# Optimization experiments

Measured on AMD Instinct MI355X. Metric: run time of the kernel, lower is better.

The kernel has to match this reference:

```python
import jax, jax.numpy as jnp
import numpy as np

N, E, G = 50000, 1600000, 64
F_NODE, F_EDGE, ACT = 128, 16, 10
NEG_SLOPE = 0.2  # GATv2Conv default negative_slope
LAYER_DIMS = [(F_NODE, 32), (32, 64), (64, 128)]


def _glorot(k, shape):
    fan_in, fan_out = shape[0], shape[-1]
    s = jnp.sqrt(6.0 / (fan_in + fan_out))
    return jax.random.uniform(k, shape, jnp.float32, -s, s)


def setup_inputs() -> dict:
    key = jax.random.key(0)
    ks = iter(jax.random.split(key, 64))
    inp = {
        "x": jax.random.normal(next(ks), (N, F_NODE), jnp.float32),
        "edge_attr": jax.random.normal(next(ks), (E, F_EDGE), jnp.float32),
        "edge_index": jax.random.randint(next(ks), (2, E), 0, N, jnp.int32),
        "batch": jnp.sort(jax.random.randint(next(ks), (N,), 0, G, jnp.int32)),
    }
    for i, (din, dout) in enumerate(LAYER_DIMS, 1):
        inp[f"Wl{i}"] = _glorot(next(ks), (din, dout))   # lin_l (source transform)
        inp[f"bl{i}"] = jnp.zeros((dout,), jnp.float32)
        inp[f"Wr{i}"] = _glorot(next(ks), (din, dout))   # lin_r (dest transform)
        inp[f"br{i}"] = jnp.zeros((dout,), jnp.float32)
        inp[f"We{i}"] = _glorot(next(ks), (F_EDGE, dout))  # lin_edge (no bias)
        inp[f"att{i}"] = _glorot(next(ks), (1, dout))[0]   # attention vector
        inp[f"bo{i}"] = jnp.zeros((dout,), jnp.float32)    # output bias
    inp["Wv1"] = _glorot(next(ks), (128, 64)); inp["bv1"] = jnp.zeros((64,), jnp.float32)
    inp["Wv2"] = _glorot(next(ks), (64, 1));   inp["bv2"] = jnp.zeros((1,), jnp.float32)
    inp["Wa1"] = _glorot(next(ks), (128, 64)); inp["ba1"] = jnp.zeros((64,), jnp.float32)
    inp["Wa2"] = _glorot(next(ks), (64, ACT)); inp["ba2"] = jnp.zeros((ACT,), jnp.float32)
    return inp


def _gatv2(x, src, dst, ea, Wl, bl, Wr, br, We, att, bo):
    """GATv2Conv, heads=1, concat=True, edge_dim=F_EDGE (eval mode)."""
    xl = x @ Wl + bl                               # [N, D] source-side
    xr = x @ Wr + br                               # [N, D] dest-side
    m = xl[src] + xr[dst] + ea @ We                # [E, D]
    score = (jax.nn.leaky_relu(m, NEG_SLOPE) * att).sum(-1)  # [E]
    # segment softmax over edges grouped by destination node
    mx = jax.lax.stop_gradient(jax.ops.segment_max(score, dst, num_segments=N))
    ex = jnp.exp(score - mx[dst])
    den = jax.ops.segment_sum(ex, dst, num_segments=N)
    alpha = ex / (den[dst] + 1e-16)                # [E]
    out = jax.ops.segment_sum(alpha[:, None] * xl[src], dst, num_segments=N)
    return out + bo


def _forward(x, edge_attr, src, dst, batch, p):
    h = x
    for i in (1, 2, 3):
        h = jax.nn.relu(_gatv2(h, src, dst, edge_attr,
                               p[f"Wl{i}"], p[f"bl{i}"], p[f"Wr{i}"], p[f"br{i}"],
                               p[f"We{i}"], p[f"att{i}"], p[f"bo{i}"]))
    # global mean pool per graph
    cnt = jax.ops.segment_sum(jnp.ones((N,), h.dtype), batch, num_segments=G)
    pooled = jax.ops.segment_sum(h, batch, num_segments=G) / jnp.maximum(cnt, 1.0)[:, None]
    # dueling heads
    v = jax.nn.relu(pooled @ p["Wv1"] + p["bv1"]) @ p["Wv2"] + p["bv2"]      # [G, 1]
    a = jax.nn.relu(pooled @ p["Wa1"] + p["ba1"]) @ p["Wa2"] + p["ba2"]      # [G, ACT]
    return v + (a - a.mean(axis=1, keepdims=True))


def reference(x, edge_attr, edge_index, batch,
              Wl1, bl1, Wr1, br1, We1, att1, bo1,
              Wl2, bl2, Wr2, br2, We2, att2, bo2,
              Wl3, bl3, Wr3, br3, We3, att3, bo3,
              Wv1, bv1, Wv2, bv2, Wa1, ba1, Wa2, ba2):
    p = dict(Wl1=Wl1, bl1=bl1, Wr1=Wr1, br1=br1, We1=We1, att1=att1, bo1=bo1,
             Wl2=Wl2, bl2=bl2, Wr2=Wr2, br2=br2, We2=We2, att2=att2, bo2=bo2,
             Wl3=Wl3, bl3=bl3, Wr3=Wr3, br3=br3, We3=We3, att3=att3, bo3=bo3,
             Wv1=Wv1, bv1=bv1, Wv2=Wv2, bv2=bv2, Wa1=Wa1, ba1=ba1, Wa2=Wa2, ba2=ba2)
    return _forward(x, edge_attr, edge_index[0], edge_index[1], batch, p)
```

## Files before the change

kernel.cpp:

```cpp
#include <hip/hip_runtime.h>
#include <cstdint>
#include <cstddef>

static constexpr int NN = 50000;
static constexpr int NE = 1600000;
static constexpr int NG = 64;
static constexpr int FE = 16;
static constexpr float SLOPE = 0.2f;

template<int DIN, int DOUT>
__global__ __launch_bounds__(256) void k_node_linear(
    const float* __restrict__ h,
    const float* __restrict__ Wl, const float* __restrict__ bl,
    const float* __restrict__ Wr, const float* __restrict__ br,
    float* __restrict__ xl, float* __restrict__ xr)
{
    __shared__ float sW[2 * DIN * DOUT];
    __shared__ float sX[16 * DIN];
    const int n0 = blockIdx.x * 16;

    for (int i = threadIdx.x; i < DIN * DOUT; i += 256) {
        sW[i] = Wl[i];
        sW[DIN * DOUT + i] = Wr[i];
    }
    for (int i = threadIdx.x; i < 16 * DIN; i += 256) {
        int r = i / DIN, k = i % DIN;
        int n = n0 + r;
        sX[i] = (n < NN) ? h[(size_t)n * DIN + k] : 0.0f;
    }
    __syncthreads();

    for (int o = threadIdx.x; o < 16 * DOUT; o += 256) {
        int r = o / DOUT, d = o % DOUT;
        int n = n0 + r;
        if (n >= NN) continue;
        float accl = bl[d], accr = br[d];
        #pragma unroll 8
        for (int k = 0; k < DIN; ++k) {
            float xv = sX[r * DIN + k];
            accl = fmaf(xv, sW[k * DOUT + d], accl);
            accr = fmaf(xv, sW[DIN * DOUT + k * DOUT + d], accr);
        }
        xl[(size_t)n * DOUT + d] = accl;
        xr[(size_t)n * DOUT + d] = accr;
    }
}

__global__ __launch_bounds__(256) void k_count(
    const int* __restrict__ ei, int* __restrict__ cnt)
{
    const int e = blockIdx.x * 256 + threadIdx.x;
    if (e >= NE) return;
    atomicAdd(cnt + ei[NE + e], 1);
}

__global__ __launch_bounds__(1024) void k_scan(
    const int* __restrict__ cnt, int* __restrict__ rowptr)
{
    __shared__ int part[1024];
    const int T = 1024;
    const int C = (NN + T - 1) / T;
    const int t = threadIdx.x;
    const int base = t * C;
    int s = 0;
    for (int i = 0; i < C; ++i) {
        int idx = base + i;
        if (idx < NN) s += cnt[idx];
    }
    part[t] = s;
    __syncthreads();
    for (int off = 1; off < T; off <<= 1) {
        int v = 0;
        if (t >= off) v = part[t - off];
        __syncthreads();
        if (t >= off) part[t] += v;
        __syncthreads();
    }
    int run = (t == 0) ? 0 : part[t - 1];
    for (int i = 0; i < C; ++i) {
        int idx = base + i;
        if (idx < NN) { rowptr[idx] = run; run += cnt[idx]; }
    }
    if (t == T - 1) rowptr[NN] = run;
}

__global__ __launch_bounds__(256) void k_fill(
    const int* __restrict__ ei, const int* __restrict__ rowptr,
    int* __restrict__ woff, int* __restrict__ eids, int* __restrict__ esrc)
{
    const int e = blockIdx.x * 256 + threadIdx.x;
    if (e >= NE) return;
    const int dst = ei[NE + e];
    const int pos = rowptr[dst] + atomicAdd(woff + dst, 1);
    eids[pos] = e;
    esrc[pos] = ei[e];
}

__global__ __launch_bounds__(256) void k_gather_ea(
    const int* __restrict__ eids, const float* __restrict__ ea,
    float* __restrict__ eap)
{
    const long long i = (long long)blockIdx.x * 256 + threadIdx.x;
    if (i >= (long long)NE * 4) return;
    const int p = (int)(i >> 2), q = (int)(i & 3);
    const int e = eids[p];
    *(float4*)(eap + (size_t)p * FE + q * 4) =
        *(const float4*)(ea + (size_t)e * FE + q * 4);
}

template<int D, bool PERM>
__global__ __launch_bounds__(128, 4) void k_gat_fused(
    const int* __restrict__ rowptr, const int* __restrict__ eidx,
    const int* __restrict__ esrc, const float* __restrict__ eaf,
    const float* __restrict__ xl, const float* __restrict__ xr,
    const float* __restrict__ We, const float* __restrict__ att,
    const float* __restrict__ bo, float* __restrict__ hout)
{
    constexpr int SW  = D / 2;
    constexpr int EPW = 64 / SW;
    constexpr int WPB = 2;

    const int wave = threadIdx.x >> 6;
    const int lane = threadIdx.x & 63;
    const int n = blockIdx.x * WPB + wave;
    if (n >= NN) return;
    const int sub = lane / SW;
    const int dl  = lane % SW;
    const int d0  = 2 * dl;

    float rWe[2 * FE], rAtt[2], rXr[2], acc[2];
    {
        const float2 a2 = *(const float2*)(att + d0);
        rAtt[0] = a2.x; rAtt[1] = a2.y;
        const float2 x2 = *(const float2*)(xr + (size_t)n * D + d0);
        rXr[0] = x2.x; rXr[1] = x2.y;
        #pragma unroll
        for (int k = 0; k < FE; ++k) {
            const float2 w2 = *(const float2*)(We + k * D + d0);
            rWe[2 * k] = w2.x; rWe[2 * k + 1] = w2.y;
        }
        acc[0] = acc[1] = 0.f;
    }

    const int p0 = rowptr[n], p1 = rowptr[n + 1];
    float m = -3.4e38f, l = 0.f;

    auto load_edge = [&](int p, float (&eav)[FE], float (&rXl)[2]) {
        const int s = esrc[p];
        const float2 x2 = *(const float2*)(xl + (size_t)s * D + d0);
        rXl[0] = x2.x; rXl[1] = x2.y;
        int erow; if constexpr (PERM) erow = p; else erow = eidx[p];
        if constexpr (SW == 64) {
            const float* ep = eaf + (size_t)(unsigned)__builtin_amdgcn_readfirstlane(erow) * FE;
            #pragma unroll
            for (int k = 0; k < FE; ++k) eav[k] = ep[k];
        } else {
            const float* ep = eaf + (size_t)erow * FE;
            #pragma unroll
            for (int k4 = 0; k4 < 4; ++k4) {
                const float4 v = *(const float4*)(ep + 4 * k4);
                eav[4 * k4]     = v.x; eav[4 * k4 + 1] = v.y;
                eav[4 * k4 + 2] = v.z; eav[4 * k4 + 3] = v.w;
            }
        }
    };
    auto score_edge = [&](const float (&eav)[FE], const float (&rXl)[2]) -> float {
        float m0 = rXl[0] + rXr[0], m1 = rXl[1] + rXr[1];
        #pragma unroll
        for (int k = 0; k < FE; ++k) {
            m0 = fmaf(eav[k], rWe[2 * k], m0);
            m1 = fmaf(eav[k], rWe[2 * k + 1], m1);
        }
        m0 = m0 > 0.f ? m0 : SLOPE * m0;
        m1 = m1 > 0.f ? m1 : SLOPE * m1;
        float sv = fmaf(m0, rAtt[0], m1 * rAtt[1]);
        #pragma unroll
        for (int off = 1; off < SW; off <<= 1) sv += __shfl_xor(sv, off);
        return sv;
    };
    auto sm_update = [&](float sv, const float (&rXl)[2]) {
        const float dd = sv - m;
        float wexp;
        if (__builtin_expect(dd > 8.f, 0)) {
            const float r = __expf(-dd);
            acc[0] *= r; acc[1] *= r;
            l *= r; m = sv; wexp = 1.f;
        } else {
            wexp = __expf(dd);
        }
        acc[0] = fmaf(wexp, rXl[0], acc[0]);
        acc[1] = fmaf(wexp, rXl[1], acc[1]);
        l += wexp;
    };

    int p = p0 + sub;
    for (; p + EPW < p1; p += 2 * EPW) {
        float eavA[FE], rXlA[2], eavB[FE], rXlB[2];
        load_edge(p, eavA, rXlA);
        load_edge(p + EPW, eavB, rXlB);
        const float svA = score_edge(eavA, rXlA);
        const float svB = score_edge(eavB, rXlB);
        sm_update(svA, rXlA);
        sm_update(svB, rXlB);
    }
    if (p < p1) {
        float eav[FE], rXl[2];
        load_edge(p, eav, rXl);
        sm_update(score_edge(eav, rXl), rXl);
    }

    #pragma unroll
    for (int step = SW; step < 64; step <<= 1) {
        const float mo = __shfl_xor(m, step);
        const float mstar = fmaxf(m, mo);
        const float sc = __expf(m - mstar);
        acc[0] *= sc; acc[1] *= sc; l *= sc;
        acc[0] += __shfl_xor(acc[0], step);
        acc[1] += __shfl_xor(acc[1], step);
        l += __shfl_xor(l, step);
        m = mstar;
    }

    if (lane < SW) {
        const float inv = 1.0f / (l + 1e-16f);
        const float2 b2 = *(const float2*)(bo + d0);
        float2 o;
        o.x = fmaxf(fmaf(acc[0], inv, b2.x), 0.f);
        o.y = fmaxf(fmaf(acc[1], inv, b2.y), 0.f);
        *(float2*)(hout + (size_t)n * D + d0) = o;
    }
}

__global__ __launch_bounds__(128) void k_pool(
    const float* __restrict__ h, const int* __restrict__ batch,
    float* __restrict__ pooled, float* __restrict__ cnt)
{
    constexpr int BLOCKS = 512;
    constexpr int CH = (NN + BLOCKS - 1) / BLOCKS;
    const int t = threadIdx.x;
    const int n0 = blockIdx.x * CH;
    const int n1 = min(NN, n0 + CH);
    if (n0 >= n1) return;

    int g = batch[n0];
    float acc = 0.f, c = 0.f;
    for (int n = n0; n < n1; ++n) {
        const int bg = batch[n];
        if (bg != g) {
            atomicAdd(pooled + g * 128 + t, acc);
            if (t == 0) atomicAdd(cnt + g, c);
            acc = 0.f; c = 0.f; g = bg;
        }
        acc += h[(size_t)n * 128 + t];
        c += 1.f;
    }
    atomicAdd(pooled + g * 128 + t, acc);
    if (t == 0) atomicAdd(cnt + g, c);
}

__global__ __launch_bounds__(128) void k_head(
    const float* __restrict__ pooled, const float* __restrict__ cnt,
    const float* __restrict__ Wv1, const float* __restrict__ bv1,
    const float* __restrict__ Wv2, const float* __restrict__ bv2,
    const float* __restrict__ Wa1, const float* __restrict__ ba1,
    const float* __restrict__ Wa2, const float* __restrict__ ba2,
    float* __restrict__ out)
{
    __shared__ float pr[128];
    __shared__ float hv[64];
    __shared__ float ha[64];
    __shared__ float sA[10];
    __shared__ float sVM[2];
    const int g = blockIdx.x;
    const int t = threadIdx.x;

    const float inv = 1.0f / fmaxf(cnt[g], 1.0f);
    pr[t] = pooled[g * 128 + t] * inv;
    __syncthreads();

    if (t < 64) {
        float sv = bv1[t], sa = ba1[t];
        #pragma unroll 8
        for (int k = 0; k < 128; ++k) {
            float p = pr[k];
            sv = fmaf(p, Wv1[k * 64 + t], sv);
            sa = fmaf(p, Wa1[k * 64 + t], sa);
        }
        hv[t] = fmaxf(sv, 0.0f);
        ha[t] = fmaxf(sa, 0.0f);
    }
    __syncthreads();

    if (t < 10) {
        float av = ba2[t];
        #pragma unroll
        for (int j = 0; j < 64; ++j) av = fmaf(ha[j], Wa2[j * 10 + t], av);
        sA[t] = av;
    }
    if (t == 64) {
        float v = bv2[0];
        #pragma unroll
        for (int j = 0; j < 64; ++j) v = fmaf(hv[j], Wv2[j], v);
        sVM[0] = v;
    }
    __syncthreads();

    if (t == 0) {
        float s = 0.0f;
        #pragma unroll
        for (int j = 0; j < 10; ++j) s += sA[j];
        sVM[1] = s * 0.1f;
    }
    __syncthreads();

    if (t < 10) out[g * 10 + t] = sVM[0] + sA[t] - sVM[1];
}

extern "C" void kernel_launch(void* const* d_in, const int* in_sizes, int n_in,
                              void* d_out, int out_size, void* d_ws, size_t ws_size,
                              hipStream_t stream)
{
    const float* x     = (const float*)d_in[0];
    const float* ea    = (const float*)d_in[1];
    const int*   ei    = (const int*)d_in[2];
    const int*   batch = (const int*)d_in[3];

    float* ws = (float*)d_ws;
    float* xl     = ws;
    float* xr     = xl + (size_t)NN * 128;
    float* hA     = xr + (size_t)NN * 128;
    float* hB     = hA + (size_t)NN * 128;
    float* pooled = hB + (size_t)NN * 64;
    float* cntp   = pooled + (size_t)NG * 128;
    int*   rowptr = (int*)(cntp + NG);
    int*   cnt    = rowptr + (NN + 1);
    int*   woff   = cnt + NN;
    int*   eids   = woff + NN;
    int*   esrc   = eids + NE;
    float* eaperm = (float*)(esrc + NE);

    const size_t need = ((char*)(eaperm + (size_t)NE * FE)) - (char*)d_ws;
    const bool use_perm = (ws_size >= need);

    const int EB = (NE + 255) / 256;

    hipMemsetAsync(cnt, 0, NN * sizeof(int), stream);
    hipMemsetAsync(woff, 0, NN * sizeof(int), stream);
    k_count<<<dim3(EB), dim3(256), 0, stream>>>(ei, cnt);
    k_scan<<<dim3(1), dim3(1024), 0, stream>>>(cnt, rowptr);
    k_fill<<<dim3(EB), dim3(256), 0, stream>>>(ei, rowptr, woff, eids, esrc);
    if (use_perm) {
        const long long tot = (long long)NE * 4;
        k_gather_ea<<<dim3((unsigned)((tot + 255) / 256)), dim3(256), 0, stream>>>(
            eids, ea, eaperm);
    }

    const int GB = (NN + 1) / 2;

#define LAYER(DIN, DOUT, HIN, HOUT, B)                                                   \
    do {                                                                                 \
        k_node_linear<DIN, DOUT><<<dim3((NN + 15) / 16), dim3(256), 0, stream>>>(        \
            HIN, (const float*)d_in[B], (const float*)d_in[(B) + 1],                     \
            (const float*)d_in[(B) + 2], (const float*)d_in[(B) + 3], xl, xr);           \
        if (use_perm)                                                                    \
            k_gat_fused<DOUT, true><<<dim3(GB), dim3(128), 0, stream>>>(                 \
                rowptr, eids, esrc, eaperm, xl, xr, (const float*)d_in[(B) + 4],         \
                (const float*)d_in[(B) + 5], (const float*)d_in[(B) + 6], HOUT);         \
        else                                                                             \
            k_gat_fused<DOUT, false><<<dim3(GB), dim3(128), 0, stream>>>(                \
                rowptr, eids, esrc, ea, xl, xr, (const float*)d_in[(B) + 4],             \
                (const float*)d_in[(B) + 5], (const float*)d_in[(B) + 6], HOUT);         \
    } while (0)

    LAYER(128, 32, x,  hA, 4);
    LAYER(32,  64, hA, hB, 11);
    LAYER(64, 128, hB, hA, 18);

#undef LAYER

    hipMemsetAsync(pooled, 0, NG * 128 * sizeof(float), stream);
    hipMemsetAsync(cntp, 0, NG * sizeof(float), stream);
    k_pool<<<dim3(512), dim3(128), 0, stream>>>(hA, batch, pooled, cntp);
    k_head<<<dim3(NG), dim3(128), 0, stream>>>(
        pooled, cntp,
        (const float*)d_in[25], (const float*)d_in[26],
        (const float*)d_in[27], (const float*)d_in[28],
        (const float*)d_in[29], (const float*)d_in[30],
        (const float*)d_in[31], (const float*)d_in[32],
        (float*)d_out);
}
```

Measured before the change: 1.000 ms.

## Fuse edge-attr permute into CSR fill, widen GAT lanes to 4 dims with packed FMA

The edge-attribute gather kernel is folded into k_fill, so each edge's 16 features are scattered straight to their CSR position, and the eids write is skipped when the permuted copy is used. That removes one launch and the eids round trip. The fused GAT kernel now gives each lane 4 output dims instead of 2, uses v_pk_fma_f32 inline asm for the edge projection, and drops the two-edge manual unroll. Adjacent memsets are merged to save launches. Wider lanes halve the shuffle reduction width but leave fewer edges in flight per wave and raise register pressure. The scatter-side ea writes are also uncoalesced.

```diff
diff --git a/kernel.cpp b/kernel.cpp
--- a/kernel.cpp
+++ b/kernel.cpp
@@ -6,7 +6,9 @@
 static constexpr int NE = 1600000;
 static constexpr int NG = 64;
 static constexpr int FE = 16;
-static constexpr float SLOPE = 0.2f;
+
+typedef float f32x2 __attribute__((ext_vector_type(2)));
+typedef float f32x4 __attribute__((ext_vector_type(4)));
 
 template<int DIN, int DOUT>
 __global__ __launch_bounds__(256) void k_node_linear(
@@ -86,26 +88,21 @@
 
 __global__ __launch_bounds__(256) void k_fill(
     const int* __restrict__ ei, const int* __restrict__ rowptr,
-    int* __restrict__ woff, int* __restrict__ eids, int* __restrict__ esrc)
+    int* __restrict__ woff, int* __restrict__ eids, int* __restrict__ esrc,
+    const float* __restrict__ ea, float* __restrict__ eaperm, const int do_perm)
 {
     const int e = blockIdx.x * 256 + threadIdx.x;
     if (e >= NE) return;
     const int dst = ei[NE + e];
     const int pos = rowptr[dst] + atomicAdd(woff + dst, 1);
-    eids[pos] = e;
     esrc[pos] = ei[e];
-}
-
-__global__ __launch_bounds__(256) void k_gather_ea(
-    const int* __restrict__ eids, const float* __restrict__ ea,
-    float* __restrict__ eap)
-{
-    const long long i = (long long)blockIdx.x * 256 + threadIdx.x;
-    if (i >= (long long)NE * 4) return;
-    const int p = (int)(i >> 2), q = (int)(i & 3);
-    const int e = eids[p];
-    *(float4*)(eap + (size_t)p * FE + q * 4) =
-        *(const float4*)(ea + (size_t)e * FE + q * 4);
+    if (do_perm) {
+        const f32x4* s4 = (const f32x4*)(ea + (size_t)e * FE);
+        f32x4* d4 = (f32x4*)(eaperm + (size_t)pos * FE);
+        d4[0] = s4[0]; d4[1] = s4[1]; d4[2] = s4[2]; d4[3] = s4[3];
+    } else {
+        eids[pos] = e;
+    }
 }
 
 template<int D, bool PERM>
@@ -116,97 +113,93 @@
     const float* __restrict__ We, const float* __restrict__ att,
     const float* __restrict__ bo, float* __restrict__ hout)
 {
-    constexpr int SW  = D / 2;
+    constexpr int SW  = D / 4;
     constexpr int EPW = 64 / SW;
-    constexpr int WPB = 2;
 
     const int wave = threadIdx.x >> 6;
     const int lane = threadIdx.x & 63;
-    const int n = blockIdx.x * WPB + wave;
+    const int n = blockIdx.x * 2 + wave;
     if (n >= NN) return;
     const int sub = lane / SW;
     const int dl  = lane % SW;
-    const int d0  = 2 * dl;
-
-    float rWe[2 * FE], rAtt[2], rXr[2], acc[2];
-    {
-        const float2 a2 = *(const float2*)(att + d0);
-        rAtt[0] = a2.x; rAtt[1] = a2.y;
-        const float2 x2 = *(const float2*)(xr + (size_t)n * D + d0);
-        rXr[0] = x2.x; rXr[1] = x2.y;
-        #pragma unroll
-        for (int k = 0; k < FE; ++k) {
-            const float2 w2 = *(const float2*)(We + k * D + d0);
-            rWe[2 * k] = w2.x; rWe[2 * k + 1] = w2.y;
-        }
-        acc[0] = acc[1] = 0.f;
-    }
-
+    const int d0  = 4 * dl;
+
+    const f32x4 rAtt = *(const f32x4*)(att + d0);
+    const f32x4 rXr  = *(const f32x4*)(xr + (size_t)n * D + d0);
+    f32x2 WeP0[8], WeP1[8], WeP2[8], WeP3[8];
+    #pragma unroll
+    for (int j = 0; j < 8; ++j) {
+        const f32x4 wa = *(const f32x4*)(We + (2 * j) * D + d0);
+        const f32x4 wb = *(const f32x4*)(We + (2 * j + 1) * D + d0);
+        WeP0[j] = (f32x2){wa.x, wb.x};
+        WeP1[j] = (f32x2){wa.y, wb.y};
+        WeP2[j] = (f32x2){wa.z, wb.z};
+        WeP3[j] = (f32x2){wa.w, wb.w};
+    }
+
+    float acc0 = 0.f, acc1 = 0.f, acc2 = 0.f, acc3 = 0.f;
+    float m = -3.4e38f, l = 0.f;
     const int p0 = rowptr[n], p1 = rowptr[n + 1];
-    float m = -3.4e38f, l = 0.f;
-
-    auto load_edge = [&](int p, float (&eav)[FE], float (&rXl)[2]) {
+
+    for (int p = p0 + sub; p < p1; p += EPW) {
         const int s = esrc[p];
-        const float2 x2 = *(const float2*)(xl + (size_t)s * D + d0);
-        rXl[0] = x2.x; rXl[1] = x2.y;
         int erow; if constexpr (PERM) erow = p; else erow = eidx[p];
-        if constexpr (SW == 64) {
-            const float* ep = eaf + (size_t)(unsigned)__builtin_amdgcn_readfirstlane(erow) * FE;
-            #pragma unroll
-            for (int k = 0; k < FE; ++k) eav[k] = ep[k];
-        } else {
-            const float* ep = eaf + (size_t)erow * FE;
-            #pragma unroll
-            for (int k4 = 0; k4 < 4; ++k4) {
-                const float4 v = *(const float4*)(ep + 4 * k4);
-                eav[4 * k4]     = v.x; eav[4 * k4 + 1] = v.y;
-                eav[4 * k4 + 2] = v.z; eav[4 * k4 + 3] = v.w;
-            }
-        }
-    };
-    auto score_edge = [&](const float (&eav)[FE], const float (&rXl)[2]) -> float {
-        float m0 = rXl[0] + rXr[0], m1 = rXl[1] + rXr[1];
-        #pragma unroll
-        for (int k = 0; k < FE; ++k) {
-            m0 = fmaf(eav[k], rWe[2 * k], m0);
-            m1 = fmaf(eav[k], rWe[2 * k + 1], m1);
-        }
-        m0 = m0 > 0.f ? m0 : SLOPE * m0;
-        m1 = m1 > 0.f ? m1 : SLOPE * m1;
-        float sv = fmaf(m0, rAtt[0], m1 * rAtt[1]);
+
+        const f32x4 xl4 = *(const f32x4*)(xl + (size_t)s * D + d0);
+        const f32x4* ep4 = (const f32x4*)(eaf + (size_t)erow * FE);
+        const f32x4 e0 = ep4[0], e1 = ep4[1], e2 = ep4[2], e3 = ep4[3];
+        f32x2 ep[8];
+        ep[0] = __builtin_shufflevector(e0, e0, 0, 1);
+        ep[1] = __builtin_shufflevector(e0, e0, 2, 3);
+        ep[2] = __builtin_shufflevector(e1, e1, 0, 1);
+        ep[3] = __builtin_shufflevector(e1, e1, 2, 3);
+        ep[4] = __builtin_shufflevector(e2, e2, 0, 1);
+        ep[5] = __builtin_shufflevector(e2, e2, 2, 3);
+        ep[6] = __builtin_shufflevector(e3, e3, 0, 1);
+        ep[7] = __builtin_shufflevector(e3, e3, 2, 3);
+
+        f32x2 q0, q1, q2, q3;
+        asm("v_pk_mul_f32 %0, %1, %2" : "=v"(q0) : "v"(WeP0[0]), "v"(ep[0]));
+        asm("v_pk_mul_f32 %0, %1, %2" : "=v"(q1) : "v"(WeP1[0]), "v"(ep[0]));
+        asm("v_pk_mul_f32 %0, %1, %2" : "=v"(q2) : "v"(WeP2[0]), "v"(ep[0]));
+        asm("v_pk_mul_f32 %0, %1, %2" : "=v"(q3) : "v"(WeP3[0]), "v"(ep[0]));
+        #pragma unroll
+        for (int j = 1; j < 8; ++j) {
+            asm("v_pk_fma_f32 %0, %1, %2, %0" : "+v"(q0) : "v"(WeP0[j]), "v"(ep[j]));
+            asm("v_pk_fma_f32 %0, %1, %2, %0" : "+v"(q1) : "v"(WeP1[j]), "v"(ep[j]));
+            asm("v_pk_fma_f32 %0, %1, %2, %0" : "+v"(q2) : "v"(WeP2[j]), "v"(ep[j]));
+            asm("v_pk_fma_f32 %0, %1, %2, %0" : "+v"(q3) : "v"(WeP3[j]), "v"(ep[j]));
+        }
+
+        float m0 = (xl4.x + rXr.x) + (q0.x + q0.y);
+        float m1 = (xl4.y + rXr.y) + (q1.x + q1.y);
+        float m2 = (xl4.z + rXr.z) + (q2.x + q2.y);
+        float m3 = (xl4.w + rXr.w) + (q3.x + q3.y);
+        m0 = fmaxf(m0, 0.2f * m0);
+        m1 = fmaxf(m1, 0.2f * m1);
+        m2 = fmaxf(m2, 0.2f * m2);
+        m3 = fmaxf(m3, 0.2f * m3);
+        float sv = m0 * rAtt.x;
+        sv = fmaf(m1, rAtt.y, sv);
+        sv = fmaf(m2, rAtt.z, sv);
+        sv = fmaf(m3, rAtt.w, sv);
         #pragma unroll
         for (int off = 1; off < SW; off <<= 1) sv += __shfl_xor(sv, off);
-        return sv;
-    };
-    auto sm_update = [&](float sv, const float (&rXl)[2]) {
+
         const float dd = sv - m;
         float wexp;
         if (__builtin_expect(dd > 8.f, 0)) {
             const float r = __expf(-dd);
-            acc[0] *= r; acc[1] *= r;
+            acc0 *= r; acc1 *= r; acc2 *= r; acc3 *= r;
             l *= r; m = sv; wexp = 1.f;
         } else {
             wexp = __expf(dd);
         }
-        acc[0] = fmaf(wexp, rXl[0], acc[0]);
-        acc[1] = fmaf(wexp, rXl[1], acc[1]);
+        acc0 = fmaf(wexp, xl4.x, acc0);
+        acc1 = fmaf(wexp, xl4.y, acc1);
+        acc2 = fmaf(wexp, xl4.z, acc2);
+        acc3 = fmaf(wexp, xl4.w, acc3);
         l += wexp;
-    };
-
-    int p = p0 + sub;
-    for (; p + EPW < p1; p += 2 * EPW) {
-        float eavA[FE], rXlA[2], eavB[FE], rXlB[2];
-        load_edge(p, eavA, rXlA);
-        load_edge(p + EPW, eavB, rXlB);
-        const float svA = score_edge(eavA, rXlA);
-        const float svB = score_edge(eavB, rXlB);
-        sm_update(svA, rXlA);
-        sm_update(svB, rXlB);
-    }
-    if (p < p1) {
-        float eav[FE], rXl[2];
-        load_edge(p, eav, rXl);
-        sm_update(score_edge(eav, rXl), rXl);
     }
 
     #pragma unroll
@@ -214,20 +207,24 @@
         const float mo = __shfl_xor(m, step);
         const float mstar = fmaxf(m, mo);
         const float sc = __expf(m - mstar);
-        acc[0] *= sc; acc[1] *= sc; l *= sc;
-        acc[0] += __shfl_xor(acc[0], step);
-        acc[1] += __shfl_xor(acc[1], step);
+        acc0 *= sc; acc1 *= sc; acc2 *= sc; acc3 *= sc; l *= sc;
+        acc0 += __shfl_xor(acc0, step);
+        acc1 += __shfl_xor(acc1, step);
+        acc2 += __shfl_xor(acc2, step);
+        acc3 += __shfl_xor(acc3, step);
         l += __shfl_xor(l, step);
         m = mstar;
     }
 
     if (lane < SW) {
         const float inv = 1.0f / (l + 1e-16f);
-        const float2 b2 = *(const float2*)(bo + d0);
-        float2 o;
-        o.x = fmaxf(fmaf(acc[0], inv, b2.x), 0.f);
-        o.y = fmaxf(fmaf(acc[1], inv, b2.y), 0.f);
-        *(float2*)(hout + (size_t)n * D + d0) = o;
+        const f32x4 b4 = *(const f32x4*)(bo + d0);
+        f32x4 o;
+        o.x = fmaxf(fmaf(acc0, inv, b4.x), 0.f);
+        o.y = fmaxf(fmaf(acc1, inv, b4.y), 0.f);
+        o.z = fmaxf(fmaf(acc2, inv, b4.z), 0.f);
+        o.w = fmaxf(fmaf(acc3, inv, b4.w), 0.f);
+        *(f32x4*)(hout + (size_t)n * D + d0) = o;
     }
 }
 
@@ -344,16 +341,11 @@
 
     const int EB = (NE + 255) / 256;
 
-    hipMemsetAsync(cnt, 0, NN * sizeof(int), stream);
-    hipMemsetAsync(woff, 0, NN * sizeof(int), stream);
+    hipMemsetAsync(cnt, 0, 2 * NN * sizeof(int), stream);
     k_count<<<dim3(EB), dim3(256), 0, stream>>>(ei, cnt);
     k_scan<<<dim3(1), dim3(1024), 0, stream>>>(cnt, rowptr);
-    k_fill<<<dim3(EB), dim3(256), 0, stream>>>(ei, rowptr, woff, eids, esrc);
-    if (use_perm) {
-        const long long tot = (long long)NE * 4;
-        k_gather_ea<<<dim3((unsigned)((tot + 255) / 256)), dim3(256), 0, stream>>>(
-            eids, ea, eaperm);
-    }
+    k_fill<<<dim3(EB), dim3(256), 0, stream>>>(
+        ei, rowptr, woff, eids, esrc, ea, eaperm, use_perm ? 1 : 0);
 
     const int GB = (NN + 1) / 2;
 
@@ -378,8 +370,7 @@
 
 #undef LAYER
 
-    hipMemsetAsync(pooled, 0, NG * 128 * sizeof(float), stream);
-    hipMemsetAsync(cntp, 0, NG * sizeof(float), stream);
+    hipMemsetAsync(pooled, 0, (NG * 128 + NG) * sizeof(float), stream);
     k_pool<<<dim3(512), dim3(128), 0, stream>>>(hA, batch, pooled, cntp);
     k_head<<<dim3(NG), dim3(128), 0, stream>>>(
         pooled, cntp,
```

Measured after the change: 1.205 ms. +20.4%, slower.
